# Kernel tuning notes

Hardware: AMD Instinct MI355X
Metric: run time of the kernel (lower is better)

Reference implementation:

```python
import jax, jax.numpy as jnp
import numpy as np

B, L, E, H = 2, 2048, 1024, 16
D = E // H

def setup_inputs() -> dict:
    key = jax.random.key(0)
    ks = jax.random.split(key, 6)
    s = 1.0 / np.sqrt(E)
    return {
        "x": jax.random.normal(ks[0], (B, L, E), dtype=jnp.float32),
        "attention_mask": jnp.ones((B, L), dtype=jnp.float32),
        "Wq": jax.random.normal(ks[1], (E, E), dtype=jnp.float32) * s,
        "Wk": jax.random.normal(ks[2], (E, E), dtype=jnp.float32) * s,
        "Wv": jax.random.normal(ks[3], (E, E), dtype=jnp.float32) * s,
        "Wo": jax.random.normal(ks[4], (E, E), dtype=jnp.float32) * s,
        "bo": jnp.zeros((E,), dtype=jnp.float32),
    }

def reference(x, attention_mask, Wq, Wk, Wv, Wo, bo):
    b, l, e = x.shape
    h, d = H, D

    def proj(W):
        # (B,L,E) @ (E,E)^T -> (B,L,E) -> (B,H,L,D)
        return (x @ W.T).reshape(b, l, h, d).transpose(0, 2, 1, 3)

    q, k, v = proj(Wq), proj(Wk), proj(Wv)

    # multiplicative attention mask on q, k, v (mask shape (B,L) -> (B,1,L,1))
    m = attention_mask[:, None, :, None].astype(x.dtype)
    q, k, v = q * m, k * m, v * m

    scale = 1.0 / np.sqrt(d)
    scores = jnp.einsum('bhqd,bhkd->bhqk', q, k) * scale  # (B,H,L,L)
    causal = jnp.tril(jnp.ones((l, l), dtype=bool))
    scores = jnp.where(causal[None, None], scores, -jnp.inf)
    attn = jax.nn.softmax(scores, axis=-1)
    y = jnp.einsum('bhqk,bhkd->bhqd', attn, v)  # (B,H,L,D)
    y = y.transpose(0, 2, 1, 3).reshape(b, l, e)
    return y @ Wo.T + bo
```

## Files before the change

kernel.cpp:

```cpp
#include <hip/hip_runtime.h>
#include <cstdint>
#include <cstddef>
#include <math.h>

#define BB 2
#define LL 2048
#define EE 1024
#define HH 16
#define DD 64
#define MM (BB*LL)

typedef short short8 __attribute__((ext_vector_type(8)));
typedef float f32x4 __attribute__((ext_vector_type(4)));
typedef float f32x16 __attribute__((ext_vector_type(16)));

#define GPTR __attribute__((address_space(1)))
#define LPTR __attribute__((address_space(3)))

__device__ __forceinline__ unsigned short f32_bf16(float f) {
  union { float f; unsigned u; } c; c.f = f;
  c.u += 0x7fffu + ((c.u >> 16) & 1u);
  return (unsigned short)(c.u >> 16);
}

__device__ __forceinline__ unsigned pk_bf16(float lo, float hi) {
  unsigned r;
  asm("v_cvt_pk_bf16_f32 %0, %1, %2" : "=v"(r) : "v"(lo), "v"(hi));
  return r;
}
__device__ __forceinline__ float ex2(float x) {
  float r;
  asm("v_exp_f32 %0, %1" : "=v"(r) : "v"(x));
  return r;
}
__device__ __forceinline__ void swap32(unsigned &a, unsigned &b) {
  asm("v_permlane32_swap_b32 %0, %1" : "+v"(a), "+v"(b));
}
__device__ __forceinline__ float xh_max(float v) {
  union { float f; unsigned u; } a, b;
  a.f = v;
  asm("v_mov_b32 %0, %1" : "=&v"(b.u) : "v"(a.u));
  asm("v_permlane32_swap_b32 %0, %1" : "+v"(a.u), "+v"(b.u));
  return fmaxf(a.f, b.f);
}
__device__ __forceinline__ float xh_sum(float v) {
  union { float f; unsigned u; } a, b;
  a.f = v;
  asm("v_mov_b32 %0, %1" : "=&v"(b.u) : "v"(a.u));
  asm("v_permlane32_swap_b32 %0, %1" : "+v"(a.u), "+v"(b.u));
  return a.f + b.f;
}
__device__ __forceinline__ f32x16 zero16() {
  f32x16 v;
  #pragma unroll
  for (int e = 0; e < 16; ++e) v[e] = 0.f;
  return v;
}

__global__ void cvt_all(const float* __restrict__ x,  const float* __restrict__ wq,
                        const float* __restrict__ wk, const float* __restrict__ wv,
                        const float* __restrict__ wo,
                        unsigned short* __restrict__ xb,  unsigned short* __restrict__ wqb,
                        unsigned short* __restrict__ wkb, unsigned short* __restrict__ wvb,
                        unsigned short* __restrict__ wob)
{
  int i = (blockIdx.x * 256 + threadIdx.x) * 4;
  if (i >= MM * EE + 4 * EE * EE) return;
  const float* s; unsigned short* d; int off;
  if (i < MM * EE) { s = x; d = xb; off = i; }
  else {
    int k = i - MM * EE;
    int w = k >> 20;
    off = k & (EE * EE - 1);
    s = (w == 0) ? wq : (w == 1) ? wk : (w == 2) ? wv : wo;
    d = (w == 0) ? wqb : (w == 1) ? wkb : (w == 2) ? wvb : wob;
  }
  float4 v = *(const float4*)(s + off);
  union { unsigned short s[4]; uint2 u; } o;
  o.s[0] = f32_bf16(v.x); o.s[1] = f32_bf16(v.y);
  o.s[2] = f32_bf16(v.z); o.s[3] = f32_bf16(v.w);
  *(uint2*)(d + off) = o.u;
}

template<int MODE>
__global__ __launch_bounds__(256, 2)
void gemm128(const unsigned short* __restrict__ A,
             const unsigned short* __restrict__ W0,
             const unsigned short* __restrict__ W1,
             const unsigned short* __restrict__ W2,
             const float* __restrict__ mask,
             const float* __restrict__ bias,
             unsigned short* __restrict__ O0,
             unsigned short* __restrict__ O1,
             unsigned short* __restrict__ O2,
             float* __restrict__ OF)
{
  constexpr int K = EE;
  const int tid = threadIdx.x;
  const int lane = tid & 63;
  const int wid = tid >> 6;
  const int g = lane >> 4, li = lane & 15;
  const int m0 = blockIdx.y * 128;
  const int n0 = blockIdx.x * 128;
  const int z = blockIdx.z;

  const unsigned short* Wp = W0;
  if (MODE == 0) Wp = (z == 0) ? W0 : ((z == 1) ? W1 : W2);

  __shared__ unsigned short As[128 * 64];
  __shared__ unsigned short Bs[128 * 64];

  f32x4 acc[4][4];
  f32x4 zero = {0.f, 0.f, 0.f, 0.f};
  #pragma unroll
  for (int i = 0; i < 4; ++i)
    #pragma unroll
    for (int j = 0; j < 4; ++j) acc[i][j] = zero;

  const int wm = (wid >> 1) * 64;
  const int wn = (wid & 1) * 64;

  for (int kt = 0; kt < K; kt += 64) {
    #pragma unroll
    for (int j = 0; j < 4; ++j) {
      int c = j * 256 + tid;
      int row = c >> 3;
      int lcol = ((c & 7) * 16) ^ ((row & 7) << 4);
      __builtin_amdgcn_global_load_lds(
        (const GPTR void*)((const char*)(A + (size_t)(m0 + row) * K + kt) + lcol),
        (LPTR void*)((char*)As + c * 16), 16, 0, 0);
      __builtin_amdgcn_global_load_lds(
        (const GPTR void*)((const char*)(Wp + (size_t)(n0 + row) * K + kt) + lcol),
        (LPTR void*)((char*)Bs + c * 16), 16, 0, 0);
    }
    __syncthreads();

    #pragma unroll
    for (int kk = 0; kk < 2; ++kk) {
      short8 a[4], b[4];
      const int colb = (kk * 32 + g * 8) * 2;
      #pragma unroll
      for (int i = 0; i < 4; ++i) {
        int ar = wm + i * 16 + li;
        a[i] = *(const short8*)((const char*)As + ar * 128 + (colb ^ ((ar & 7) << 4)));
        int br = wn + i * 16 + li;
        b[i] = *(const short8*)((const char*)Bs + br * 128 + (colb ^ ((br & 7) << 4)));
      }
      #pragma unroll
      for (int i = 0; i < 4; ++i)
        #pragma unroll
        for (int j = 0; j < 4; ++j)
          acc[i][j] = __builtin_amdgcn_mfma_f32_16x16x32_bf16(a[i], b[j], acc[i][j], 0, 0, 0);
    }
    __syncthreads();
  }

  if (MODE == 0) {
    if (z == 2) {
      #pragma unroll
      for (int i = 0; i < 4; ++i) {
        int mbase = m0 + wm + i * 16 + g * 4;
        int bb2 = mbase >> 11;
        int l0  = mbase & (LL - 1);
        float mk[4];
        #pragma unroll
        for (int r = 0; r < 4; ++r) mk[r] = mask[mbase + r];
        #pragma unroll
        for (int j = 0; j < 4; ++j) {
          int n = n0 + wn + j * 16 + li;
          int h2 = n >> 6, dd2 = n & 63;
          union { unsigned short s[4]; uint2 u; } o;
          #pragma unroll
          for (int r = 0; r < 4; ++r) o.s[r] = f32_bf16(acc[i][j][r] * mk[r]);
          size_t off = (size_t)(bb2 * HH + h2) * (LL * DD)
                     + (size_t)(l0 >> 5) * (DD * 32) + dd2 * 32 + (l0 & 31);
          *(uint2*)(O2 + off) = o.u;
        }
      }
    } else {
      unsigned short* Op = (z == 0) ? O0 : O1;
      const float sc = (z == 0) ? 0.125f * 1.44269504088896f : 1.0f;
      #pragma unroll
      for (int i = 0; i < 4; ++i) {
        #pragma unroll
        for (int r = 0; r < 4; ++r) {
          int m = m0 + wm + i * 16 + g * 4 + r;
          float mk = mask[m] * sc;
          int bb = m >> 11;
          int l  = m & (LL - 1);
          #pragma unroll
          for (int j = 0; j < 4; ++j) {
            int n = n0 + wn + j * 16 + li;
            int h = n >> 6, d = n & 63;
            size_t off = (((size_t)(bb * HH + h)) * LL + l) * DD + d;
            Op[off] = f32_bf16(acc[i][j][r] * mk);
          }
        }
      }
    }
  } else {
    #pragma unroll
    for (int i = 0; i < 4; ++i) {
      #pragma unroll
      for (int j = 0; j < 4; ++j) {
        int n = n0 + wn + j * 16 + li;
        float bv = bias[n];
        #pragma unroll
        for (int r = 0; r < 4; ++r) {
          int m = m0 + wm + i * 16 + g * 4 + r;
          OF[(size_t)m * EE + n] = acc[i][j][r] + bv;
        }
      }
    }
  }
}

__global__ __launch_bounds__(128, 2)
void attn8(const unsigned short* __restrict__ Q,
           const unsigned short* __restrict__ K,
           const unsigned short* __restrict__ VT,
           unsigned short* __restrict__ Y)
{
  const int tid = threadIdx.x, lane = tid & 63, w = tid >> 6;
  const int l31 = lane & 31, hi = lane >> 5;

  const int id = blockIdx.x;
  const int lo = id & 7;
  const int r_ = id >> 3;
  const int bh = (r_ & 3) * 8 + lo;
  const int p  = r_ >> 2;
  const int qth = 63 - p;
  const int qtl = p;
  const int b = bh >> 4, h = bh & (HH - 1);
  const size_t kbase = (size_t)bh * LL * DD;

  const unsigned short* Kg  = K + kbase;
  const unsigned short* VTg = VT + kbase;

  const int qrh = qth * 32 + l31;
  const int qrl = qtl * 32 + l31;

  short8 qfh[4], qfl[4];
  {
    const unsigned short* Qr = Q + kbase + (size_t)qrh * DD + hi * 8;
    #pragma unroll
    for (int kc = 0; kc < 4; ++kc) qfh[kc] = *(const short8*)(Qr + kc * 16);
    const unsigned short* Qs = Q + kbase + (size_t)qrl * DD + hi * 8;
    #pragma unroll
    for (int kc = 0; kc < 4; ++kc) qfl[kc] = *(const short8*)(Qs + kc * 16);
  }

  const f32x16 kZero = zero16();
  f32x16 oh0 = zero16(), oh1 = zero16(), ol0 = zero16(), ol1 = zero16();
  float mh = -INFINITY, lsh = 0.f, ml = -INFINITY, lsl = 0.f;

  short8 kA[4], vA[4], kB[4], vB[4];

  auto loadtile = [&](short8 (&kk)[4], short8 (&vv)[4], int t2) {
    const int kv0 = t2 << 5;
    const unsigned short* Kp = Kg + ((size_t)(kv0 + l31) << 6) + hi * 8;
    #pragma unroll
    for (int kc = 0; kc < 4; ++kc) kk[kc] = *(const short8*)(Kp + kc * 16);
    const unsigned short* Vp = VTg + (size_t)(kv0 >> 5) * (DD * 32) + l31 * 32 + hi * 8;
    vv[0] = *(const short8*)(Vp);
    vv[1] = *(const short8*)(Vp + 16);
    vv[2] = *(const short8*)(Vp + 32 * 32);
    vv[3] = *(const short8*)(Vp + 32 * 32 + 16);
  };

  loadtile(kA, vA, w);

  auto qk = [&](const short8 (&ck)[4], const short8 (&qf)[4]) -> f32x16 {
    __builtin_amdgcn_s_setprio(1);
    f32x16 s = __builtin_amdgcn_mfma_f32_32x32x16_bf16(ck[0], qf[0], kZero, 0, 0, 0);
    #pragma unroll
    for (int kc = 1; kc < 4; ++kc)
      s = __builtin_amdgcn_mfma_f32_32x32x16_bf16(ck[kc], qf[kc], s, 0, 0, 0);
    __builtin_amdgcn_s_setprio(0);
    return s;
  };

  auto process = [&](f32x16 &s, const short8 (&cv)[4],
                     float &mq, float &lq, f32x16 &o0, f32x16 &o1) {
    float r0 = fmaxf(fmaxf(fmaxf(s[0], s[8]),  fmaxf(s[1], s[9])),  fmaxf(s[2], s[10]));
    float r1 = fmaxf(fmaxf(fmaxf(s[3], s[11]), fmaxf(s[4], s[12])), fmaxf(s[5], s[13]));
    float r2 = fmaxf(fmaxf(s[6], s[14]), fmaxf(s[7], s[15]));
    float mv = xh_max(fmaxf(fmaxf(r0, r1), r2));

    if (!__all(mv <= mq + 8.0f)) {
      float mnew = fmaxf(mq, mv);
      float al = ex2(mq - mnew);
      mq = mnew;
      lq *= al;
      #pragma unroll
      for (int e = 0; e < 16; ++e) { o0[e] *= al; o1[e] *= al; }
    }

    float ra[8];
    #pragma unroll
    for (int e = 0; e < 16; ++e) s[e] = ex2(s[e] - mq);
    #pragma unroll
    for (int e = 0; e < 8; ++e) ra[e] = s[e] + s[e + 8];
    #pragma unroll
    for (int st = 4; st >= 1; st >>= 1)
      #pragma unroll
      for (int e = 0; e < 4; ++e) if (e < st) ra[e] += ra[e + st];
    lq += xh_sum(ra[0]);

    auto mkfrag = [&](int base) -> short8 {
      unsigned a0 = pk_bf16(s[base + 0], s[base + 1]);
      unsigned a1 = pk_bf16(s[base + 2], s[base + 3]);
      unsigned b0 = pk_bf16(s[base + 4], s[base + 5]);
      unsigned b1 = pk_bf16(s[base + 6], s[base + 7]);
      swap32(a0, b0);
      swap32(a1, b1);
      union { unsigned u[4]; short8 s8; } f;
      f.u[0] = a0; f.u[1] = a1; f.u[2] = b0; f.u[3] = b1;
      return f.s8;
    };
    short8 pf0 = mkfrag(0), pf1 = mkfrag(8);

    __builtin_amdgcn_s_setprio(1);
    o0 = __builtin_amdgcn_mfma_f32_32x32x16_bf16(cv[0], pf0, o0, 0, 0, 0);
    o0 = __builtin_amdgcn_mfma_f32_32x32x16_bf16(cv[1], pf1, o0, 0, 0, 0);
    o1 = __builtin_amdgcn_mfma_f32_32x32x16_bf16(cv[2], pf0, o1, 0, 0, 0);
    o1 = __builtin_amdgcn_mfma_f32_32x32x16_bf16(cv[3], pf1, o1, 0, 0, 0);
    __builtin_amdgcn_s_setprio(0);
  };

  auto body = [&](short8 (&ck)[4], short8 (&cv)[4],
                  short8 (&nk)[4], short8 (&nv)[4], int t) {
    if (t + 2 <= qth) loadtile(nk, nv, t + 2);

    {
      f32x16 s = qk(ck, qfh);
      if (t == qth) {
        #pragma unroll
        for (int i = 0; i < 16; ++i) {
          int kvr = (i & 3) + 8 * (i >> 2) + 4 * hi;
          if (kvr > l31) s[i] = -INFINITY;
        }
      }
      process(s, cv, mh, lsh, oh0, oh1);
    }
    if (t <= qtl) {
      f32x16 s = qk(ck, qfl);
      if (t == qtl) {
        #pragma unroll
        for (int i = 0; i < 16; ++i) {
          int kvr = (i & 3) + 8 * (i >> 2) + 4 * hi;
          if (kvr > l31) s[i] = -INFINITY;
        }
      }
      process(s, cv, ml, lsl, ol0, ol1);
    }
  };

  for (int t = w; t <= qth; t += 4) {
    body(kA, vA, kB, vB, t);
    if (t + 2 <= qth) body(kB, vB, kA, vA, t + 2);
  }

  __shared__ float mg[2][64][34];
  if (w == 1) {
    mg[0][lane][0] = mh; mg[0][lane][1] = lsh;
    mg[1][lane][0] = ml; mg[1][lane][1] = lsl;
    #pragma unroll
    for (int e = 0; e < 16; ++e) {
      mg[0][lane][2 + e] = oh0[e]; mg[0][lane][18 + e] = oh1[e];
      mg[1][lane][2 + e] = ol0[e]; mg[1][lane][18 + e] = ol1[e];
    }
  }
  __syncthreads();
  if (w == 0) {
    #pragma unroll
    for (int q = 0; q < 2; ++q) {
      float mw = (q == 0) ? mh : ml;
      float lw = (q == 0) ? lsh : lsl;
      const f32x16& o0 = (q == 0) ? oh0 : ol0;
      const f32x16& o1 = (q == 0) ? oh1 : ol1;
      int qrow = (q == 0) ? qrh : qrl;
      float m1 = mg[q][lane][0], l1 = mg[q][lane][1];
      float M = fmaxf(mw, m1);
      float a0 = ex2(fmaxf(mw - M, -200.0f));
      float a1 = ex2(fmaxf(m1 - M, -200.0f));
      float Lt = lw * a0 + l1 * a1;
      float inv = 1.0f / Lt;
      unsigned short* Yr = Y + ((size_t)b * LL + qrow) * EE + h * DD;
      #pragma unroll
      for (int rg = 0; rg < 4; ++rg) {
        union { unsigned short s[4]; uint2 u; } u0, u1;
        #pragma unroll
        for (int e = 0; e < 4; ++e) {
          int i = rg * 4 + e;
          u0.s[e] = f32_bf16((o0[i] * a0 + mg[q][lane][2 + i]  * a1) * inv);
          u1.s[e] = f32_bf16((o1[i] * a0 + mg[q][lane][18 + i] * a1) * inv);
        }
        *(uint2*)(Yr + rg * 8 + hi * 4) = u0.u;
        *(uint2*)(Yr + 32 + rg * 8 + hi * 4) = u1.u;
      }
    }
  }
}

extern "C" void kernel_launch(void* const* d_in, const int* in_sizes, int n_in,
                              void* d_out, int out_size, void* d_ws, size_t ws_size,
                              hipStream_t stream) {
  const float* x    = (const float*)d_in[0];
  const float* mask = (const float*)d_in[1];
  const float* Wq   = (const float*)d_in[2];
  const float* Wk   = (const float*)d_in[3];
  const float* Wv   = (const float*)d_in[4];
  const float* Wo   = (const float*)d_in[5];
  const float* bo   = (const float*)d_in[6];
  float* out = (float*)d_out;

  char* ws = (char*)d_ws;
  unsigned short* xb  = (unsigned short*)(ws);
  unsigned short* wqb = (unsigned short*)(ws + ((size_t)8  << 20));
  unsigned short* wkb = (unsigned short*)(ws + ((size_t)10 << 20));
  unsigned short* wvb = (unsigned short*)(ws + ((size_t)12 << 20));
  unsigned short* wob = (unsigned short*)(ws + ((size_t)14 << 20));
  unsigned short* Qb  = (unsigned short*)(ws + ((size_t)16 << 20));
  unsigned short* Kb  = (unsigned short*)(ws + ((size_t)24 << 20));
  unsigned short* VTb = (unsigned short*)(ws + ((size_t)32 << 20));
  unsigned short* Yb  = (unsigned short*)(ws + ((size_t)40 << 20));

  cvt_all<<<8192, 256, 0, stream>>>(x, Wq, Wk, Wv, Wo, xb, wqb, wkb, wvb, wob);

  gemm128<0><<<dim3(EE / 128, MM / 128, 3), 256, 0, stream>>>(
      xb, wqb, wkb, wvb, mask, nullptr, Qb, Kb, VTb, nullptr);

  attn8<<<dim3(1024), 128, 0, stream>>>(Qb, Kb, VTb, Yb);

  gemm128<1><<<dim3(EE / 128, MM / 128, 1), 256, 0, stream>>>(
      Yb, wob, nullptr, nullptr, nullptr, bo, nullptr, nullptr, nullptr, out);
}
```

Measured before the change: 109.0 us.

## Process KV tiles in pairs of 64 keys per online-softmax step

The attention kernel now loads and processes two 32-key tiles per iteration, doing one max/rescale/sum reduction over 64 keys instead of two 32-key reductions. This halves the per-tile softmax bookkeeping (cross-lane max and sum, rescale checks) and issues larger batches of loads and MFMAs. The PV MFMAs are also interleaved across the two output accumulators to break dependency chains. In exchange it roughly doubles the K/V fragment registers held for double-buffering, which may pressure occupancy under the two-blocks launch bound, and it adds branches for the diagonal and odd-tile cases.

```diff
diff --git a/kernel.cpp b/kernel.cpp
--- a/kernel.cpp
+++ b/kernel.cpp
@@ -216,7 +216,7 @@
 }
 
 __global__ __launch_bounds__(128, 2)
-void attn8(const unsigned short* __restrict__ Q,
+void attn9(const unsigned short* __restrict__ Q,
            const unsigned short* __restrict__ K,
            const unsigned short* __restrict__ VT,
            unsigned short* __restrict__ Y)
@@ -254,21 +254,28 @@
   f32x16 oh0 = zero16(), oh1 = zero16(), ol0 = zero16(), ol1 = zero16();
   float mh = -INFINITY, lsh = 0.f, ml = -INFINITY, lsl = 0.f;
 
-  short8 kA[4], vA[4], kB[4], vB[4];
-
-  auto loadtile = [&](short8 (&kk)[4], short8 (&vv)[4], int t2) {
-    const int kv0 = t2 << 5;
-    const unsigned short* Kp = Kg + ((size_t)(kv0 + l31) << 6) + hi * 8;
-    #pragma unroll
-    for (int kc = 0; kc < 4; ++kc) kk[kc] = *(const short8*)(Kp + kc * 16);
-    const unsigned short* Vp = VTg + (size_t)(kv0 >> 5) * (DD * 32) + l31 * 32 + hi * 8;
-    vv[0] = *(const short8*)(Vp);
-    vv[1] = *(const short8*)(Vp + 16);
-    vv[2] = *(const short8*)(Vp + 32 * 32);
-    vv[3] = *(const short8*)(Vp + 32 * 32 + 16);
-  };
-
-  loadtile(kA, vA, w);
+  short8 kA0[4], kA1[4], vA0[4], vA1[4];
+  short8 kB0[4], kB1[4], vB0[4], vB1[4];
+
+  auto loadpair = [&](short8 (&k0)[4], short8 (&k1)[4],
+                      short8 (&v0)[4], short8 (&v1)[4], int pt) {
+    const int t0 = pt << 1;
+    const unsigned short* Kp = Kg + ((size_t)(t0 * 32 + l31) << 6) + hi * 8;
+    #pragma unroll
+    for (int kc = 0; kc < 4; ++kc) {
+      k0[kc] = *(const short8*)(Kp + kc * 16);
+      k1[kc] = *(const short8*)(Kp + 2048 + kc * 16);
+    }
+    const unsigned short* Vp = VTg + (size_t)t0 * (DD * 32) + l31 * 32 + hi * 8;
+    v0[0] = *(const short8*)(Vp);
+    v0[1] = *(const short8*)(Vp + 16);
+    v0[2] = *(const short8*)(Vp + 1024);
+    v0[3] = *(const short8*)(Vp + 1024 + 16);
+    v1[0] = *(const short8*)(Vp + 2048);
+    v1[1] = *(const short8*)(Vp + 2048 + 16);
+    v1[2] = *(const short8*)(Vp + 2048 + 1024);
+    v1[3] = *(const short8*)(Vp + 2048 + 1024 + 16);
+  };
 
   auto qk = [&](const short8 (&ck)[4], const short8 (&qf)[4]) -> f32x16 {
     __builtin_amdgcn_s_setprio(1);
@@ -280,8 +287,28 @@
     return s;
   };
 
-  auto process = [&](f32x16 &s, const short8 (&cv)[4],
-                     float &mq, float &lq, f32x16 &o0, f32x16 &o1) {
+  auto diagmask = [&](f32x16 &s) {
+    #pragma unroll
+    for (int i = 0; i < 16; ++i) {
+      int kvr = (i & 3) + 8 * (i >> 2) + 4 * hi;
+      if (kvr > l31) s[i] = -INFINITY;
+    }
+  };
+
+  auto mkfrag = [&](const f32x16 &s, int base) -> short8 {
+    unsigned a0 = pk_bf16(s[base + 0], s[base + 1]);
+    unsigned a1 = pk_bf16(s[base + 2], s[base + 3]);
+    unsigned b0 = pk_bf16(s[base + 4], s[base + 5]);
+    unsigned b1 = pk_bf16(s[base + 6], s[base + 7]);
+    swap32(a0, b0);
+    swap32(a1, b1);
+    union { unsigned u[4]; short8 s8; } f;
+    f.u[0] = a0; f.u[1] = a1; f.u[2] = b0; f.u[3] = b1;
+    return f.s8;
+  };
+
+  auto process32 = [&](f32x16 &s, const short8 (&cv)[4],
+                       float &mq, float &lq, f32x16 &o0, f32x16 &o1) {
     float r0 = fmaxf(fmaxf(fmaxf(s[0], s[8]),  fmaxf(s[1], s[9])),  fmaxf(s[2], s[10]));
     float r1 = fmaxf(fmaxf(fmaxf(s[3], s[11]), fmaxf(s[4], s[12])), fmaxf(s[5], s[13]));
     float r2 = fmaxf(fmaxf(s[6], s[14]), fmaxf(s[7], s[15]));
@@ -307,58 +334,109 @@
       for (int e = 0; e < 4; ++e) if (e < st) ra[e] += ra[e + st];
     lq += xh_sum(ra[0]);
 
-    auto mkfrag = [&](int base) -> short8 {
-      unsigned a0 = pk_bf16(s[base + 0], s[base + 1]);
-      unsigned a1 = pk_bf16(s[base + 2], s[base + 3]);
-      unsigned b0 = pk_bf16(s[base + 4], s[base + 5]);
-      unsigned b1 = pk_bf16(s[base + 6], s[base + 7]);
-      swap32(a0, b0);
-      swap32(a1, b1);
-      union { unsigned u[4]; short8 s8; } f;
-      f.u[0] = a0; f.u[1] = a1; f.u[2] = b0; f.u[3] = b1;
-      return f.s8;
-    };
-    short8 pf0 = mkfrag(0), pf1 = mkfrag(8);
+    short8 pf0 = mkfrag(s, 0), pf1 = mkfrag(s, 8);
 
     __builtin_amdgcn_s_setprio(1);
     o0 = __builtin_amdgcn_mfma_f32_32x32x16_bf16(cv[0], pf0, o0, 0, 0, 0);
+    o1 = __builtin_amdgcn_mfma_f32_32x32x16_bf16(cv[2], pf0, o1, 0, 0, 0);
     o0 = __builtin_amdgcn_mfma_f32_32x32x16_bf16(cv[1], pf1, o0, 0, 0, 0);
-    o1 = __builtin_amdgcn_mfma_f32_32x32x16_bf16(cv[2], pf0, o1, 0, 0, 0);
     o1 = __builtin_amdgcn_mfma_f32_32x32x16_bf16(cv[3], pf1, o1, 0, 0, 0);
     __builtin_amdgcn_s_setprio(0);
   };
 
-  auto body = [&](short8 (&ck)[4], short8 (&cv)[4],
-                  short8 (&nk)[4], short8 (&nv)[4], int t) {
-    if (t + 2 <= qth) loadtile(nk, nv, t + 2);
+  auto process64 = [&](f32x16 &sa, f32x16 &sb,
+                       const short8 (&cva)[4], const short8 (&cvb)[4],
+                       float &mq, float &lq, f32x16 &o0, f32x16 &o1) {
+    float red[8];
+    #pragma unroll
+    for (int e = 0; e < 8; ++e)
+      red[e] = fmaxf(fmaxf(sa[e], sa[e + 8]), fmaxf(sb[e], sb[e + 8]));
+    #pragma unroll
+    for (int st = 4; st >= 1; st >>= 1)
+      #pragma unroll
+      for (int e = 0; e < 4; ++e) if (e < st) red[e] = fmaxf(red[e], red[e + st]);
+    float mv = xh_max(red[0]);
+
+    if (!__all(mv <= mq + 8.0f)) {
+      float mnew = fmaxf(mq, mv);
+      float al = ex2(mq - mnew);
+      mq = mnew;
+      lq *= al;
+      #pragma unroll
+      for (int e = 0; e < 16; ++e) { o0[e] *= al; o1[e] *= al; }
+    }
+
+    #pragma unroll
+    for (int e = 0; e < 16; ++e) sa[e] = ex2(sa[e] - mq);
+    #pragma unroll
+    for (int e = 0; e < 16; ++e) sb[e] = ex2(sb[e] - mq);
+    float ra[8];
+    #pragma unroll
+    for (int e = 0; e < 8; ++e) ra[e] = (sa[e] + sa[e + 8]) + (sb[e] + sb[e + 8]);
+    #pragma unroll
+    for (int st = 4; st >= 1; st >>= 1)
+      #pragma unroll
+      for (int e = 0; e < 4; ++e) if (e < st) ra[e] += ra[e + st];
+    lq += xh_sum(ra[0]);
+
+    short8 pfA0 = mkfrag(sa, 0), pfA1 = mkfrag(sa, 8);
+    short8 pfB0 = mkfrag(sb, 0), pfB1 = mkfrag(sb, 8);
+
+    __builtin_amdgcn_s_setprio(1);
+    o0 = __builtin_amdgcn_mfma_f32_32x32x16_bf16(cva[0], pfA0, o0, 0, 0, 0);
+    o1 = __builtin_amdgcn_mfma_f32_32x32x16_bf16(cva[2], pfA0, o1, 0, 0, 0);
+    o0 = __builtin_amdgcn_mfma_f32_32x32x16_bf16(cva[1], pfA1, o0, 0, 0, 0);
+    o1 = __builtin_amdgcn_mfma_f32_32x32x16_bf16(cva[3], pfA1, o1, 0, 0, 0);
+    o0 = __builtin_amdgcn_mfma_f32_32x32x16_bf16(cvb[0], pfB0, o0, 0, 0, 0);
+    o1 = __builtin_amdgcn_mfma_f32_32x32x16_bf16(cvb[2], pfB0, o1, 0, 0, 0);
+    o0 = __builtin_amdgcn_mfma_f32_32x32x16_bf16(cvb[1], pfB1, o0, 0, 0, 0);
+    o1 = __builtin_amdgcn_mfma_f32_32x32x16_bf16(cvb[3], pfB1, o1, 0, 0, 0);
+    __builtin_amdgcn_s_setprio(0);
+  };
+
+  auto body = [&](short8 (&ck0)[4], short8 (&ck1)[4],
+                  short8 (&cv0)[4], short8 (&cv1)[4],
+                  short8 (&nk0)[4], short8 (&nk1)[4],
+                  short8 (&nv0)[4], short8 (&nv1)[4], int pt) {
+    if (2 * (pt + 2) <= qth) loadpair(nk0, nk1, nv0, nv1, pt + 2);
+    const int t0 = pt << 1, t1 = t0 + 1;
 
     {
-      f32x16 s = qk(ck, qfh);
-      if (t == qth) {
-        #pragma unroll
-        for (int i = 0; i < 16; ++i) {
-          int kvr = (i & 3) + 8 * (i >> 2) + 4 * hi;
-          if (kvr > l31) s[i] = -INFINITY;
-        }
-      }
-      process(s, cv, mh, lsh, oh0, oh1);
-    }
-    if (t <= qtl) {
-      f32x16 s = qk(ck, qfl);
-      if (t == qtl) {
-        #pragma unroll
-        for (int i = 0; i < 16; ++i) {
-          int kvr = (i & 3) + 8 * (i >> 2) + 4 * hi;
-          if (kvr > l31) s[i] = -INFINITY;
-        }
-      }
-      process(s, cv, ml, lsl, ol0, ol1);
-    }
-  };
-
-  for (int t = w; t <= qth; t += 4) {
-    body(kA, vA, kB, vB, t);
-    if (t + 2 <= qth) body(kB, vB, kA, vA, t + 2);
+      f32x16 sa = qk(ck0, qfh);
+      if (t1 < qth) {
+        f32x16 sb = qk(ck1, qfh);
+        process64(sa, sb, cv0, cv1, mh, lsh, oh0, oh1);
+      } else if (t1 == qth) {
+        f32x16 sb = qk(ck1, qfh);
+        diagmask(sb);
+        process64(sa, sb, cv0, cv1, mh, lsh, oh0, oh1);
+      } else {
+        diagmask(sa);
+        process32(sa, cv0, mh, lsh, oh0, oh1);
+      }
+    }
+    if (t0 <= qtl) {
+      f32x16 sa = qk(ck0, qfl);
+      if (t1 < qtl) {
+        f32x16 sb = qk(ck1, qfl);
+        process64(sa, sb, cv0, cv1, ml, lsl, ol0, ol1);
+      } else if (t1 == qtl) {
+        f32x16 sb = qk(ck1, qfl);
+        diagmask(sb);
+        process64(sa, sb, cv0, cv1, ml, lsl, ol0, ol1);
+      } else {
+        diagmask(sa);
+        process32(sa, cv0, ml, lsl, ol0, ol1);
+      }
+    }
+  };
+
+  loadpair(kA0, kA1, vA0, vA1, w);
+
+  for (int pt = w; 2 * pt <= qth; pt += 4) {
+    body(kA0, kA1, vA0, vA1, kB0, kB1, vB0, vB1, pt);
+    if (2 * (pt + 2) <= qth)
+      body(kB0, kB1, vB0, vB1, kA0, kA1, vA0, vA1, pt + 2);
   }
 
   __shared__ float mg[2][64][34];
@@ -431,7 +509,7 @@
   gemm128<0><<<dim3(EE / 128, MM / 128, 3), 256, 0, stream>>>(
       xb, wqb, wkb, wvb, mask, nullptr, Qb, Kb, VTb, nullptr);
 
-  attn8<<<dim3(1024), 128, 0, stream>>>(Qb, Kb, VTb, Yb);
+  attn9<<<dim3(1024), 128, 0, stream>>>(Qb, Kb, VTb, Yb);
 
   gemm128<1><<<dim3(EE / 128, MM / 128, 1), 256, 0, stream>>>(
       Yb, wob, nullptr, nullptr, nullptr, bo, nullptr, nullptr, nullptr, out);
```

After: 126.6 us. 1.16x slower.
